# Performance work log

Measured on AMD Instinct MI355X. Metric: run time of the kernel, lower is better.

Reference implementation:

```python
import math
import jax, jax.numpy as jnp
import numpy as np

HEADS = 16
MASKED_BIAS = -10000.0


def setup_inputs() -> dict:
    key = jax.random.key(0)
    kq, kk, kv = jax.random.split(key, 3)
    B, S, D = 4, 1024, 2048
    q = jax.random.normal(kq, (B, S, D), dtype=jnp.float32)
    k = jax.random.normal(kk, (B, S, D), dtype=jnp.float32)
    v = jax.random.normal(kv, (B, S, D), dtype=jnp.float32)
    return {"q": q, "k": k, "v": v}


def _mha(q, k, v):
    B, Sq, D = q.shape
    Sk = k.shape[-2]
    hd = D // HEADS
    # (B, H, S, hd)
    qh = q.reshape(B, Sq, HEADS, hd).transpose(0, 2, 1, 3)
    kh = k.reshape(B, Sk, HEADS, hd).transpose(0, 2, 1, 3)
    vh = v.reshape(B, Sk, HEADS, hd).transpose(0, 2, 1, 3)
    scores = jnp.einsum("bhqd,bhkd->bhqk", qh, kh) / math.sqrt(hd)
    # causal mask: query i attends to keys <= i (aligned to end of kv)
    qi = jnp.arange(Sq)[:, None] + (Sk - Sq)
    ki = jnp.arange(Sk)[None, :]
    causal = ki <= qi  # (Sq, Sk)
    scores = jnp.where(causal[None, None], scores, jnp.asarray(MASKED_BIAS, scores.dtype))
    attn = jax.nn.softmax(scores, axis=-1)
    out = jnp.einsum("bhqk,bhkd->bhqd", attn, vh)
    return out.transpose(0, 2, 1, 3).reshape(B, Sq, D)


def reference(q, k, v):
    return _mha(q, k, v)
```

## Files before the change

### kernel.cpp

```cpp
#include <hip/hip_runtime.h>
#include <hip/hip_bf16.h>


#define HEADS  16
#define HD     128
#define SEQ    1024
#define DMODEL 2048

typedef _Float16 f16;
typedef __attribute__((ext_vector_type(8))) _Float16 f16x8;
typedef __attribute__((ext_vector_type(4))) _Float16 f16x4;
typedef __attribute__((ext_vector_type(4))) float    f32x4;
typedef __attribute__((ext_vector_type(4))) unsigned int u32x4;

#define KSTR 136
#define VSTR 72

__device__ __forceinline__ unsigned int pkrtz(float a, float b) {
    return __builtin_bit_cast(unsigned int, __builtin_amdgcn_cvt_pkrtz(a, b));
}

__global__ __launch_bounds__(256, 2)
void fa_fwd(const float* __restrict__ Q,
            const float* __restrict__ K,
            const float* __restrict__ V,
            float* __restrict__ O)
{
    __shared__ f16 kT[64 * KSTR];
    __shared__ f16 vT[HD * VSTR];

    const int tid  = threadIdx.x;
    const int lane = tid & 63;
    const int wv   = tid >> 6;
    const int quad = lane >> 4;
    const int cl   = lane & 15;

    const int bh = blockIdx.x;
    const int qt = 15 - blockIdx.y;
    const int qb = qt * 64;
    const long long head_off = ((long long)(bh >> 4) * SEQ) * DMODEL
                             + (long long)(bh & 15) * HD;
    const float rscale = 0.08838834764831845f;

    const int krow = tid >> 4;
    const int kcol = (tid & 15) * 8;
    const int vr0  = (tid & 31) * 2;
    const int vcg  = tid >> 5;

    f32x4 kraw[8], vraw[8];
    unsigned int kpk[16], vpk[16];

    auto loadK = [&](int kbase) {
        #pragma unroll
        for (int i = 0; i < 4; ++i) {
            const float* kp = K + head_off + (long long)(kbase + krow + i * 16) * DMODEL + kcol;
            kraw[2 * i]     = *(const f32x4*)kp;
            kraw[2 * i + 1] = *(const f32x4*)(kp + 4);
        }
    };
    auto packK = [&]() {
        #pragma unroll
        for (int i = 0; i < 8; ++i) {
            kpk[2 * i]     = pkrtz(kraw[i][0], kraw[i][1]);
            kpk[2 * i + 1] = pkrtz(kraw[i][2], kraw[i][3]);
        }
    };
    auto loadV = [&](int kbase) {
        const float* vp = V + head_off + (long long)(kbase + vr0) * DMODEL + vcg * 16;
        #pragma unroll
        for (int j = 0; j < 4; ++j) {
            vraw[j]     = *(const f32x4*)(vp + 4 * j);
            vraw[4 + j] = *(const f32x4*)(vp + DMODEL + 4 * j);
        }
    };
    auto packV = [&]() {
        #pragma unroll
        for (int j = 0; j < 16; ++j)
            vpk[j] = pkrtz(vraw[j >> 2][j & 3], vraw[4 + (j >> 2)][j & 3]);
    };

    const int qrow = qb + wv * 16 + cl;
    f16x8 qf[4];
    {
        const float* qp = Q + head_off + (long long)qrow * DMODEL + quad * 8;
        #pragma unroll
        for (int kk = 0; kk < 4; ++kk) {
            f32x4 qa = *(const f32x4*)(qp + kk * 32);
            f32x4 qc = *(const f32x4*)(qp + kk * 32 + 4);
            union { f16x8 v; unsigned int u[4]; } qw;
            qw.u[0] = pkrtz(qa[0], qa[1]);
            qw.u[1] = pkrtz(qa[2], qa[3]);
            qw.u[2] = pkrtz(qc[0], qc[1]);
            qw.u[3] = pkrtz(qc[2], qc[3]);
            qf[kk] = qw.v;
        }
    }

    f32x4 acc[8];
    #pragma unroll
    for (int i = 0; i < 8; ++i) acc[i] = (f32x4){0.f, 0.f, 0.f, 0.f};
    float ls = 0.f;

    loadK(0);
    loadV(0);
    packK();
    packV();

    #pragma unroll 1
    for (int kt = 0; kt <= qt; ++kt) {
        const int kbase = kt * 64;

        __syncthreads();
        #pragma unroll
        for (int i = 0; i < 4; ++i)
            *(u32x4*)&kT[(krow + i * 16) * KSTR + kcol] = *(u32x4*)&kpk[4 * i];
        #pragma unroll
        for (int j = 0; j < 16; ++j)
            *(unsigned int*)&vT[(vcg * 16 + j) * VSTR + vr0] = vpk[j];
        __syncthreads();

        const bool more = (kt < qt);
        if (more) loadK(kbase + 64);

        f32x4 sc[4];
        #pragma unroll
        for (int st = 0; st < 4; ++st) sc[st] = (f32x4){0.f, 0.f, 0.f, 0.f};
        #pragma unroll
        for (int kk = 0; kk < 4; ++kk) {
            #pragma unroll
            for (int st = 0; st < 4; ++st) {
                f16x8 kf = *(const f16x8*)&kT[(st * 16 + cl) * KSTR + kk * 32 + quad * 8];
                sc[st] = __builtin_amdgcn_mfma_f32_16x16x32_f16(kf, qf[kk], sc[st], 0, 0, 0);
            }
        }

        if (more) packK();

        f16x4 pf[4];
        if (kt == qt) {
            #pragma unroll
            for (int st = 0; st < 4; ++st) {
                float e[4];
                #pragma unroll
                for (int r = 0; r < 4; ++r) {
                    int key = kbase + st * 16 + quad * 4 + r;
                    float ex = __expf(sc[st][r] * rscale);
                    e[r] = (key <= qrow) ? ex : 0.f;
                    ls += e[r];
                }
                union { f16x4 v; unsigned int u[2]; } pw;
                pw.u[0] = pkrtz(e[0], e[1]);
                pw.u[1] = pkrtz(e[2], e[3]);
                pf[st] = pw.v;
            }
        } else {
            #pragma unroll
            for (int st = 0; st < 4; ++st) {
                float e[4];
                #pragma unroll
                for (int r = 0; r < 4; ++r) {
                    e[r] = __expf(sc[st][r] * rscale);
                    ls += e[r];
                }
                union { f16x4 v; unsigned int u[2]; } pw;
                pw.u[0] = pkrtz(e[0], e[1]);
                pw.u[1] = pkrtz(e[2], e[3]);
                pf[st] = pw.v;
            }
        }

        if (more) loadV(kbase + 64);

        #pragma unroll
        for (int dt = 0; dt < 8; ++dt) {
            #pragma unroll
            for (int st = 0; st < 4; ++st) {
                f16x4 vf = *(const f16x4*)&vT[(dt * 16 + cl) * VSTR + st * 16 + quad * 4];
                acc[dt] = __builtin_amdgcn_mfma_f32_16x16x16f16(vf, pf[st], acc[dt], 0, 0, 0);
            }
        }

        if (more) packV();
    }

    float lsum = ls;
    lsum += __shfl_xor(lsum, 16, 64);
    lsum += __shfl_xor(lsum, 32, 64);
    const float rl = 1.0f / lsum;

    float* op = O + head_off + (long long)qrow * DMODEL + quad * 4;
    #pragma unroll
    for (int dt = 0; dt < 8; ++dt) {
        f32x4 o4 = acc[dt];
        o4[0] *= rl; o4[1] *= rl; o4[2] *= rl; o4[3] *= rl;
        *(f32x4*)(op + dt * 16) = o4;
    }
}

extern "C" void kernel_launch(void* const* d_in, const int* in_sizes, int n_in,
                              void* d_out, int out_size, void* d_ws, size_t ws_size,
                              hipStream_t stream) {
    const float* q = (const float*)d_in[0];
    const float* k = (const float*)d_in[1];
    const float* v = (const float*)d_in[2];
    float* o = (float*)d_out;

    dim3 grid(4 * HEADS, SEQ / 64);
    dim3 block(256);
    fa_fwd<<<grid, block, 0, stream>>>(q, k, v, o);
}
```

Baseline: 171.9 us.

## Swizzle K/V shared tiles with XOR instead of padding, prefetch K and V together

Replaces the padded shared-memory strides for the K and transposed V tiles with XOR-swizzled unpadded layouts, which avoids bank conflicts while using less LDS. It also merges the K and V global prefetches into a single call issued right after the barrier, and moves the fp16 packing into the LDS store phase so the packed register arrays are no longer kept live. The trade-off is that V's global loads are now issued earlier and held in registers across the QK and PV MMA phases, which raises register pressure. The swizzle also adds address arithmetic to every LDS access.

```diff
diff --git a/kernel.cpp b/kernel.cpp
--- a/kernel.cpp
+++ b/kernel.cpp
@@ -13,9 +13,6 @@
 typedef __attribute__((ext_vector_type(4))) float    f32x4;
 typedef __attribute__((ext_vector_type(4))) unsigned int u32x4;
 
-#define KSTR 136
-#define VSTR 72
-
 __device__ __forceinline__ unsigned int pkrtz(float a, float b) {
     return __builtin_bit_cast(unsigned int, __builtin_amdgcn_cvt_pkrtz(a, b));
 }
@@ -26,8 +23,8 @@
             const float* __restrict__ V,
             float* __restrict__ O)
 {
-    __shared__ f16 kT[64 * KSTR];
-    __shared__ f16 vT[HD * VSTR];
+    __shared__ f16 kT[64 * 128];
+    __shared__ f16 vT[128 * 64];
 
     const int tid  = threadIdx.x;
     const int lane = tid & 63;
@@ -43,40 +40,28 @@
     const float rscale = 0.08838834764831845f;
 
     const int krow = tid >> 4;
-    const int kcol = (tid & 15) * 8;
+    const int kg   = tid & 15;
+    const int kgs  = kg ^ krow;
     const int vr0  = (tid & 31) * 2;
     const int vcg  = tid >> 5;
+    const int vg   = vr0 >> 3;
+    const int vo   = vr0 & 7;
 
     f32x4 kraw[8], vraw[8];
-    unsigned int kpk[16], vpk[16];
 
-    auto loadK = [&](int kbase) {
+    auto loadKV = [&](int kbase) {
         #pragma unroll
         for (int i = 0; i < 4; ++i) {
-            const float* kp = K + head_off + (long long)(kbase + krow + i * 16) * DMODEL + kcol;
+            const float* kp = K + head_off + (long long)(kbase + krow + i * 16) * DMODEL + kg * 8;
             kraw[2 * i]     = *(const f32x4*)kp;
             kraw[2 * i + 1] = *(const f32x4*)(kp + 4);
         }
-    };
-    auto packK = [&]() {
-        #pragma unroll
-        for (int i = 0; i < 8; ++i) {
-            kpk[2 * i]     = pkrtz(kraw[i][0], kraw[i][1]);
-            kpk[2 * i + 1] = pkrtz(kraw[i][2], kraw[i][3]);
-        }
-    };
-    auto loadV = [&](int kbase) {
         const float* vp = V + head_off + (long long)(kbase + vr0) * DMODEL + vcg * 16;
         #pragma unroll
         for (int j = 0; j < 4; ++j) {
             vraw[j]     = *(const f32x4*)(vp + 4 * j);
             vraw[4 + j] = *(const f32x4*)(vp + DMODEL + 4 * j);
         }
-    };
-    auto packV = [&]() {
-        #pragma unroll
-        for (int j = 0; j < 16; ++j)
-            vpk[j] = pkrtz(vraw[j >> 2][j & 3], vraw[4 + (j >> 2)][j & 3]);
     };
 
     const int qrow = qb + wv * 16 + cl;
@@ -101,26 +86,29 @@
     for (int i = 0; i < 8; ++i) acc[i] = (f32x4){0.f, 0.f, 0.f, 0.f};
     float ls = 0.f;
 
-    loadK(0);
-    loadV(0);
-    packK();
-    packV();
+    loadKV(0);
 
     #pragma unroll 1
     for (int kt = 0; kt <= qt; ++kt) {
-        const int kbase = kt * 64;
-
-        __syncthreads();
-        #pragma unroll
-        for (int i = 0; i < 4; ++i)
-            *(u32x4*)&kT[(krow + i * 16) * KSTR + kcol] = *(u32x4*)&kpk[4 * i];
-        #pragma unroll
-        for (int j = 0; j < 16; ++j)
-            *(unsigned int*)&vT[(vcg * 16 + j) * VSTR + vr0] = vpk[j];
         __syncthreads();
 
-        const bool more = (kt < qt);
-        if (more) loadK(kbase + 64);
+        #pragma unroll
+        for (int i = 0; i < 4; ++i) {
+            u32x4 w;
+            w.x = pkrtz(kraw[2 * i][0], kraw[2 * i][1]);
+            w.y = pkrtz(kraw[2 * i][2], kraw[2 * i][3]);
+            w.z = pkrtz(kraw[2 * i + 1][0], kraw[2 * i + 1][1]);
+            w.w = pkrtz(kraw[2 * i + 1][2], kraw[2 * i + 1][3]);
+            *(u32x4*)&kT[(krow + 16 * i) * 128 + kgs * 8] = w;
+        }
+        #pragma unroll
+        for (int j = 0; j < 16; ++j) {
+            unsigned int pk = pkrtz(vraw[j >> 2][j & 3], vraw[4 + (j >> 2)][j & 3]);
+            *(unsigned int*)&vT[(vcg * 16 + j) * 64 + ((vg ^ (j & 7)) * 8) + vo] = pk;
+        }
+        __syncthreads();
+
+        if (kt < qt) loadKV((kt + 1) * 64);
 
         f32x4 sc[4];
         #pragma unroll
@@ -129,13 +117,13 @@
         for (int kk = 0; kk < 4; ++kk) {
             #pragma unroll
             for (int st = 0; st < 4; ++st) {
-                f16x8 kf = *(const f16x8*)&kT[(st * 16 + cl) * KSTR + kk * 32 + quad * 8];
+                f16x8 kf = *(const f16x8*)&kT[(st * 16 + cl) * 128
+                                              + ((kk * 4 + quad) ^ cl) * 8];
                 sc[st] = __builtin_amdgcn_mfma_f32_16x16x32_f16(kf, qf[kk], sc[st], 0, 0, 0);
             }
         }
 
-        if (more) packK();
-
+        const int kbase = kt * 64;
         f16x4 pf[4];
         if (kt == qt) {
             #pragma unroll
@@ -169,18 +157,16 @@
             }
         }
 
-        if (more) loadV(kbase + 64);
-
         #pragma unroll
         for (int dt = 0; dt < 8; ++dt) {
             #pragma unroll
             for (int st = 0; st < 4; ++st) {
-                f16x4 vf = *(const f16x4*)&vT[(dt * 16 + cl) * VSTR + st * 16 + quad * 4];
+                f16x4 vf = *(const f16x4*)&vT[(dt * 16 + cl) * 64
+                                              + ((st * 2 + (quad >> 1)) ^ (cl & 7)) * 8
+                                              + (quad & 1) * 4];
                 acc[dt] = __builtin_amdgcn_mfma_f32_16x16x16f16(vf, pf[st], acc[dt], 0, 0, 0);
             }
         }
-
-        if (more) packV();
     }
 
     float lsum = ls;
```

After: 169.7 us. No clear change (-1.3%).
